# Kernel tuning notes

Measured on AMD Instinct MI355X. Metric: run time of the kernel, lower is better.

The kernel has to match this reference:

```python
import jax, jax.numpy as jnp
import numpy as np

D_X = 1024
D_TEXT = 768
FUSION_DIM = D_X + D_TEXT  # 1792
M = 16
K = 2


def setup_inputs() -> dict:
    key = jax.random.key(0)
    k1, k2, k3, k4, k5 = jax.random.split(key, 5)
    B, H, W = 256, 32, 32
    x = jax.random.normal(k1, (B, D_X, H, W), dtype=jnp.float32)
    degraded = jax.random.normal(k2, (B, D_TEXT), dtype=jnp.float32)
    # learned params (random so routing is non-trivial)
    w_fusion = jax.random.normal(k3, (FUSION_DIM, FUSION_DIM), dtype=jnp.float32) * (1.0 / np.sqrt(FUSION_DIM))
    b_fusion = jax.random.normal(k4, (FUSION_DIM,), dtype=jnp.float32) * 0.01
    w_gate = jax.random.normal(k5, (FUSION_DIM, M), dtype=jnp.float32) * 0.02
    return {"x": x, "degraded": degraded, "w_fusion": w_fusion,
            "b_fusion": b_fusion, "w_gate": w_gate}


def reference(x, degraded, w_fusion, b_fusion, w_gate):
    B = x.shape[0]
    # global average pool over H,W -> [B, d_x]
    x_pooled = jnp.mean(x, axis=(2, 3))
    fused = jnp.concatenate([x_pooled, degraded], axis=1)        # [B, d_x+d_text]
    fused = jnp.dot(fused, w_fusion) + b_fusion                  # Linear
    fused = jax.nn.gelu(fused, approximate=False)                # exact GELU (torch default)
    clean_logits = jnp.dot(fused, w_gate)                        # [B, M]
    probs_for_mi = jax.nn.softmax(clean_logits, axis=1)
    # eval path: logits = clean_logits (no noise)
    num_consider = min(K + 1, M)
    top_logits, top_indices = jax.lax.top_k(clean_logits, num_consider)
    top_k_logits = top_logits[:, :K]
    top_k_indices = top_indices[:, :K]
    top_k_gates = jax.nn.softmax(top_k_logits, axis=1)
    rows = jnp.arange(B)[:, None]
    gates = jnp.zeros_like(clean_logits).at[rows, top_k_indices].set(top_k_gates)
    moe_loss = jnp.float32(0.0)
    return gates, moe_loss, probs_for_mi, top_k_indices
```

## Files before the change

### kernel.cpp

```cpp
#include <hip/hip_runtime.h>
#include <math.h>

#define D_X      1024
#define D_TEXT   768
#define FDIM     1792
#define BATCH    256
#define M_EXP    16
#define HW_TOT   1024

#define OUT_GATES 0
#define OUT_LOSS  4096
#define OUT_PROBS 4097
#define OUT_IDX   8193

#define NBLK_DGEMM 224
#define NBLK_POOL  (BATCH * D_X / 4)

__global__ __launch_bounds__(256) void pool_deggemm_kernel(const float* __restrict__ x,
                                                           const float* __restrict__ deg,
                                                           const float* __restrict__ W,
                                                           float* __restrict__ fused,
                                                           float* __restrict__ pact2) {
    __shared__ float As1[32][33];
    __shared__ float Ws1[32][64];

    const int bid = blockIdx.x;
    const int tid = threadIdx.x;

    if (bid >= NBLK_DGEMM) {
        const int gtid = (bid - NBLK_DGEMM) * 256 + tid;
        const int row  = gtid >> 6;
        const int lane = gtid & 63;
        const float4* xr = reinterpret_cast<const float4*>(x + (size_t)row * HW_TOT);
        float s = 0.0f;
#pragma unroll
        for (int k = 0; k < 4; ++k) {
            float4 v = xr[k * 64 + lane];
            s += v.x + v.y + v.z + v.w;
        }
#pragma unroll
        for (int off = 32; off > 0; off >>= 1) s += __shfl_xor(s, off, 64);
        if (lane == 0) fused[row] = s * (1.0f / 1024.0f);
        return;
    }

    const int mb = bid / 28;
    const int nb = bid % 28;
    const int m0 = mb * 32;
    const int n0 = nb * 64;

    const int tx = tid & 15;
    const int ty = tid >> 4;

    const int ar  = tid >> 3;
    const int ak4 = (tid & 7) * 4;
    const int wk  = tid >> 4;
    const int wc4 = (tid & 15) * 4;

    float acc[2][4] = {};

    for (int k0 = 0; k0 < D_TEXT; k0 += 32) {
        __syncthreads();
        {
            const float4 a = *reinterpret_cast<const float4*>(
                deg + (size_t)(m0 + ar) * D_TEXT + k0 + ak4);
            As1[ak4 + 0][ar] = a.x; As1[ak4 + 1][ar] = a.y;
            As1[ak4 + 2][ar] = a.z; As1[ak4 + 3][ar] = a.w;
            *reinterpret_cast<float4*>(&Ws1[wk][wc4]) =
                *reinterpret_cast<const float4*>(W + (size_t)(D_X + k0 + wk) * FDIM + n0 + wc4);
            *reinterpret_cast<float4*>(&Ws1[wk + 16][wc4]) =
                *reinterpret_cast<const float4*>(W + (size_t)(D_X + k0 + wk + 16) * FDIM + n0 + wc4);
        }
        __syncthreads();
#pragma unroll
        for (int kk = 0; kk < 32; ++kk) {
            const float2 a = *reinterpret_cast<const float2*>(&As1[kk][ty * 2]);
            const float4 w = *reinterpret_cast<const float4*>(&Ws1[kk][tx * 4]);
            acc[0][0] = fmaf(a.x, w.x, acc[0][0]);
            acc[0][1] = fmaf(a.x, w.y, acc[0][1]);
            acc[0][2] = fmaf(a.x, w.z, acc[0][2]);
            acc[0][3] = fmaf(a.x, w.w, acc[0][3]);
            acc[1][0] = fmaf(a.y, w.x, acc[1][0]);
            acc[1][1] = fmaf(a.y, w.y, acc[1][1]);
            acc[1][2] = fmaf(a.y, w.z, acc[1][2]);
            acc[1][3] = fmaf(a.y, w.w, acc[1][3]);
        }
    }

#pragma unroll
    for (int i = 0; i < 2; ++i) {
        float4 v;
        v.x = acc[i][0]; v.y = acc[i][1]; v.z = acc[i][2]; v.w = acc[i][3];
        *reinterpret_cast<float4*>(pact2 + (size_t)(m0 + ty * 2 + i) * FDIM + n0 + tx * 4) = v;
    }
}

#define BM 32
#define BN 64
#define BK 64
#define KDIM D_X
#define NITER (KDIM / BK)
#define ASTR 36

#define AS(buf, k, m) As[(buf) * 2304 + (k) * ASTR + (m)]
#define WS(buf, k, n) Ws[(buf) * 4096 + (k) * 64 + (n)]
#define PACC(w, m, n) smem[(w) * 2048 + (m) * 64 + (n)]
#define ACTS(m, n)    smem[8192 + (m) * 65 + (n)]
#define WGS(n, e)     smem[10272 + (n) * M_EXP + (e)]

#define LOADA(k0)                                                                            \
    pa0 = *reinterpret_cast<const float4*>(A + (size_t)(m0 + ar) * KDIM + (k0) + ak4);       \
    pa1 = *reinterpret_cast<const float4*>(A + (size_t)(m0 + ar + 16) * KDIM + (k0) + ak4);

#define LOADW(k0)                                                                            \
    pw0 = *reinterpret_cast<const float4*>(W + (size_t)((k0) + wr0) * FDIM + n0 + wc4);      \
    pw1 = *reinterpret_cast<const float4*>(W + (size_t)((k0) + wr0 + 16) * FDIM + n0 + wc4); \
    pw2 = *reinterpret_cast<const float4*>(W + (size_t)((k0) + wr0 + 32) * FDIM + n0 + wc4); \
    pw3 = *reinterpret_cast<const float4*>(W + (size_t)((k0) + wr0 + 48) * FDIM + n0 + wc4);

#define STOREA(buf)                                                                          \
    AS(buf, ak4 + 0, ar) = pa0.x; AS(buf, ak4 + 1, ar) = pa0.y;                              \
    AS(buf, ak4 + 2, ar) = pa0.z; AS(buf, ak4 + 3, ar) = pa0.w;                              \
    AS(buf, ak4 + 0, ar + 16) = pa1.x; AS(buf, ak4 + 1, ar + 16) = pa1.y;                    \
    AS(buf, ak4 + 2, ar + 16) = pa1.z; AS(buf, ak4 + 3, ar + 16) = pa1.w;

#define STOREW(buf)                                                                          \
    *reinterpret_cast<float4*>(&WS(buf, wr0, wc4))      = pw0;                               \
    *reinterpret_cast<float4*>(&WS(buf, wr0 + 16, wc4)) = pw1;                               \
    *reinterpret_cast<float4*>(&WS(buf, wr0 + 32, wc4)) = pw2;                               \
    *reinterpret_cast<float4*>(&WS(buf, wr0 + 48, wc4)) = pw3;

__global__ __launch_bounds__(256) void gemm_gate_kernel(const float* __restrict__ A,
                                                        const float* __restrict__ W,
                                                        const float* __restrict__ pact2,
                                                        const float* __restrict__ bias,
                                                        const float* __restrict__ wg,
                                                        float* __restrict__ part,
                                                        int* __restrict__ done,
                                                        float* __restrict__ out) {
    __shared__ float smem[12800];
    __shared__ int isLast;
    float* As = smem;
    float* Ws = smem + 4608;

    const int tid = threadIdx.x;
    const int m0 = blockIdx.x * BM;
    const int n0 = blockIdx.y * BN;

    const int ar  = tid >> 4;
    const int ak4 = (tid & 15) * 4;
    const int wr0 = tid >> 4;
    const int wc4 = (tid & 15) * 4;

    const int wv   = tid >> 6;
    const int lane = tid & 63;
    const int mg   = lane >> 3;
    const int ng   = lane & 7;

    float4 pa0, pa1, pw0, pw1, pw2, pw3;

    LOADA(0); LOADW(0);
    STOREA(0); STOREW(0);
    LOADA(BK); LOADW(BK);
    __syncthreads();

    float acc[4][8] = {};
    int cur = 0;

    for (int t = 0; t < NITER; ++t) {
#pragma unroll
        for (int s = 0; s < 16; ++s) {
            const int kk = wv * 16 + s;
            const float4 a  = *reinterpret_cast<const float4*>(&AS(cur, kk, mg * 4));
            const float4 w0 = *reinterpret_cast<const float4*>(&WS(cur, kk, ng * 8));
            const float4 w1 = *reinterpret_cast<const float4*>(&WS(cur, kk, ng * 8 + 4));
            const float av[4] = {a.x, a.y, a.z, a.w};
            const float wvv[8] = {w0.x, w0.y, w0.z, w0.w, w1.x, w1.y, w1.z, w1.w};
#pragma unroll
            for (int i = 0; i < 4; ++i)
#pragma unroll
                for (int j = 0; j < 8; ++j)
                    acc[i][j] = fmaf(av[i], wvv[j], acc[i][j]);
        }
        if (t < NITER - 1) {
            const int nxt = cur ^ 1;
            STOREA(nxt); STOREW(nxt);
            if (t < NITER - 2) {
                const int k0 = (t + 2) * BK;
                LOADA(k0); LOADW(k0);
            }
            __syncthreads();
            cur = nxt;
        }
    }

    __syncthreads();

#pragma unroll
    for (int i = 0; i < 4; ++i) {
        float4 v0, v1;
        v0.x = acc[i][0]; v0.y = acc[i][1]; v0.z = acc[i][2]; v0.w = acc[i][3];
        v1.x = acc[i][4]; v1.y = acc[i][5]; v1.z = acc[i][6]; v1.w = acc[i][7];
        *reinterpret_cast<float4*>(&PACC(wv, mg * 4 + i, ng * 8))     = v0;
        *reinterpret_cast<float4*>(&PACC(wv, mg * 4 + i, ng * 8 + 4)) = v1;
    }
    {
        const int r  = tid >> 2;
        const int c4 = (tid & 3) * 4;
        *reinterpret_cast<float4*>(&WGS(r, c4)) =
            *reinterpret_cast<const float4*>(wg + (size_t)(n0 + r) * M_EXP + c4);
    }
    __syncthreads();

    {
        const int m   = tid >> 3;
        const int nb8 = (tid & 7) * 8;
#pragma unroll
        for (int h = 0; h < 2; ++h) {
            const int n = nb8 + h * 4;
            const float4 p  = *reinterpret_cast<const float4*>(
                pact2 + (size_t)(m0 + m) * FDIM + n0 + n);
            const float4 bb = *reinterpret_cast<const float4*>(bias + n0 + n);
            const float pv[4] = {p.x, p.y, p.z, p.w};
            const float bv[4] = {bb.x, bb.y, bb.z, bb.w};
#pragma unroll
            for (int j = 0; j < 4; ++j) {
                const float v = ((PACC(0, m, n + j) + PACC(1, m, n + j))
                               + (PACC(2, m, n + j) + PACC(3, m, n + j)))
                               + pv[j] + bv[j];
                ACTS(m, n + j) = v * 0.5f * (1.0f + erff(v * 0.70710678118654752440f));
            }
        }
    }
    __syncthreads();

    const int pm = tid >> 3;
    const int pe = (tid & 7) * 2;
    float s0 = 0.0f, s1 = 0.0f;
#pragma unroll
    for (int n = 0; n < BN; ++n) {
        const float a = ACTS(pm, n);
        s0 = fmaf(a, WGS(n, pe), s0);
        s1 = fmaf(a, WGS(n, pe + 1), s1);
    }
    float* pr = part + ((size_t)blockIdx.y * BATCH + m0 + pm) * M_EXP + pe;
    pr[0] = s0;
    pr[1] = s1;

    __threadfence();
    __syncthreads();
    if (tid == 0) {
        const int prev = __hip_atomic_fetch_add(done, 1, __ATOMIC_ACQ_REL,
                                                __HIP_MEMORY_SCOPE_AGENT);
        isLast = (prev == 8 * 28 - 1);
    }
    __syncthreads();
    if (!isLast) return;

    {
        const int b = tid;
        float l[M_EXP];
#pragma unroll
        for (int m = 0; m < M_EXP; ++m) l[m] = 0.0f;
        for (int nb2 = 0; nb2 < FDIM / BN; ++nb2) {
            const float4* prr = reinterpret_cast<const float4*>(
                part + ((size_t)nb2 * BATCH + b) * M_EXP);
#pragma unroll
            for (int q = 0; q < 4; ++q) {
                const float4 v = prr[q];
                l[q * 4 + 0] += v.x;
                l[q * 4 + 1] += v.y;
                l[q * 4 + 2] += v.z;
                l[q * 4 + 3] += v.w;
            }
        }
        float mx = l[0];
#pragma unroll
        for (int m = 1; m < M_EXP; ++m) mx = fmaxf(mx, l[m]);
        float e[M_EXP], s = 0.0f;
#pragma unroll
        for (int m = 0; m < M_EXP; ++m) { e[m] = expf(l[m] - mx); s += e[m]; }
        const float inv = 1.0f / s;
#pragma unroll
        for (int m = 0; m < M_EXP; ++m) out[OUT_PROBS + b * M_EXP + m] = e[m] * inv;

        int i0 = 0; float v0 = l[0];
#pragma unroll
        for (int m = 1; m < M_EXP; ++m) if (l[m] > v0) { v0 = l[m]; i0 = m; }
        int i1 = -1; float v1 = -INFINITY;
#pragma unroll
        for (int m = 0; m < M_EXP; ++m) if (m != i0 && l[m] > v1) { v1 = l[m]; i1 = m; }

        const float t = expf(v1 - v0);
        const float g0 = 1.0f / (1.0f + t);
        const float g1 = t * g0;
#pragma unroll
        for (int m = 0; m < M_EXP; ++m) out[OUT_GATES + b * M_EXP + m] = 0.0f;
        out[OUT_GATES + b * M_EXP + i0] = g0;
        out[OUT_GATES + b * M_EXP + i1] = g1;
        out[OUT_IDX + b * 2 + 0] = (float)i0;
        out[OUT_IDX + b * 2 + 1] = (float)i1;
        if (b == 0) out[OUT_LOSS] = 0.0f;
    }
}

extern "C" void kernel_launch(void* const* d_in, const int* in_sizes, int n_in,
                              void* d_out, int out_size, void* d_ws, size_t ws_size,
                              hipStream_t stream) {
    const float* x        = (const float*)d_in[0];
    const float* degraded = (const float*)d_in[1];
    const float* w_fusion = (const float*)d_in[2];
    const float* b_fusion = (const float*)d_in[3];
    const float* w_gate   = (const float*)d_in[4];
    float* out = (float*)d_out;

    float* fused = (float*)d_ws;
    float* pact2 = fused + (size_t)BATCH * D_X;
    float* part  = pact2 + (size_t)BATCH * FDIM;
    int*   done  = (int*)(part + (size_t)28 * BATCH * M_EXP);

    hipMemsetAsync(done, 0, sizeof(int), stream);

    pool_deggemm_kernel<<<NBLK_DGEMM + NBLK_POOL, 256, 0, stream>>>(x, degraded, w_fusion,
                                                                   fused, pact2);

    gemm_gate_kernel<<<dim3(BATCH / BM, FDIM / BN), 256, 0, stream>>>(fused, w_fusion, pact2,
                                                                     b_fusion, w_gate, part,
                                                                     done, out);
}
```

Baseline: 234.3 us.

## Split-K the pooled-feature GEMM across two blocks with per-tile completion counters

The main GEMM over the pooled x features is split into two K halves via a third grid dimension, doubling block count from 224 to 448. Each half writes partial sums to a global workspace, and a per-tile atomic counter lets the second finisher sum both halves, add the bias and degraded contribution, apply GELU, and run the gate projection. The intra-block 4-wave K split with shared-memory reduction is replaced by a simpler 2x4 per-thread tile. The aim is better CU occupancy on a small grid, at the cost of extra global traffic for partials and an added atomic synchronization.

```diff
diff --git a/kernel.cpp b/kernel.cpp
--- a/kernel.cpp
+++ b/kernel.cpp
@@ -98,15 +98,14 @@
 #define BM 32
 #define BN 64
 #define BK 64
+#define KHALF 512
+#define NITER (KHALF / BK)
 #define KDIM D_X
-#define NITER (KDIM / BK)
-#define ASTR 36
-
-#define AS(buf, k, m) As[(buf) * 2304 + (k) * ASTR + (m)]
-#define WS(buf, k, n) Ws[(buf) * 4096 + (k) * 64 + (n)]
-#define PACC(w, m, n) smem[(w) * 2048 + (m) * 64 + (n)]
-#define ACTS(m, n)    smem[8192 + (m) * 65 + (n)]
-#define WGS(n, e)     smem[10272 + (n) * M_EXP + (e)]
+
+#define AS(buf, k, m) smem[(buf) * 2112 + (k) * 33 + (m)]
+#define WS(buf, k, n) smem[4224 + (buf) * 4096 + (k) * 64 + (n)]
+#define ACTS(m, n)    smem[(m) * 65 + (n)]
+#define WGS(n, e)     smem[2080 + (n) * M_EXP + (e)]
 
 #define LOADA(k0)                                                                            \
     pa0 = *reinterpret_cast<const float4*>(A + (size_t)(m0 + ar) * KDIM + (k0) + ak4);       \
@@ -135,58 +134,56 @@
                                                         const float* __restrict__ pact2,
                                                         const float* __restrict__ bias,
                                                         const float* __restrict__ wg,
+                                                        float* __restrict__ pactz,
                                                         float* __restrict__ part,
+                                                        int* __restrict__ tilectr,
                                                         int* __restrict__ done,
                                                         float* __restrict__ out) {
-    __shared__ float smem[12800];
-    __shared__ int isLast;
-    float* As = smem;
-    float* Ws = smem + 4608;
+    __shared__ float smem[12416];
+    __shared__ int isL;
 
     const int tid = threadIdx.x;
     const int m0 = blockIdx.x * BM;
     const int n0 = blockIdx.y * BN;
-
+    const int z  = blockIdx.z;
+    const int kz = z * KHALF;
+
+    const int tx = tid & 15;
+    const int ty = tid >> 4;
     const int ar  = tid >> 4;
     const int ak4 = (tid & 15) * 4;
     const int wr0 = tid >> 4;
     const int wc4 = (tid & 15) * 4;
 
-    const int wv   = tid >> 6;
-    const int lane = tid & 63;
-    const int mg   = lane >> 3;
-    const int ng   = lane & 7;
-
     float4 pa0, pa1, pw0, pw1, pw2, pw3;
 
-    LOADA(0); LOADW(0);
+    LOADA(kz); LOADW(kz);
     STOREA(0); STOREW(0);
-    LOADA(BK); LOADW(BK);
-    __syncthreads();
-
-    float acc[4][8] = {};
+    LOADA(kz + BK); LOADW(kz + BK);
+    __syncthreads();
+
+    float acc[2][4] = {};
     int cur = 0;
 
     for (int t = 0; t < NITER; ++t) {
 #pragma unroll
-        for (int s = 0; s < 16; ++s) {
-            const int kk = wv * 16 + s;
-            const float4 a  = *reinterpret_cast<const float4*>(&AS(cur, kk, mg * 4));
-            const float4 w0 = *reinterpret_cast<const float4*>(&WS(cur, kk, ng * 8));
-            const float4 w1 = *reinterpret_cast<const float4*>(&WS(cur, kk, ng * 8 + 4));
-            const float av[4] = {a.x, a.y, a.z, a.w};
-            const float wvv[8] = {w0.x, w0.y, w0.z, w0.w, w1.x, w1.y, w1.z, w1.w};
-#pragma unroll
-            for (int i = 0; i < 4; ++i)
-#pragma unroll
-                for (int j = 0; j < 8; ++j)
-                    acc[i][j] = fmaf(av[i], wvv[j], acc[i][j]);
+        for (int kk = 0; kk < BK; ++kk) {
+            const float2 a = *reinterpret_cast<const float2*>(&AS(cur, kk, ty * 2));
+            const float4 w = *reinterpret_cast<const float4*>(&WS(cur, kk, tx * 4));
+            acc[0][0] = fmaf(a.x, w.x, acc[0][0]);
+            acc[0][1] = fmaf(a.x, w.y, acc[0][1]);
+            acc[0][2] = fmaf(a.x, w.z, acc[0][2]);
+            acc[0][3] = fmaf(a.x, w.w, acc[0][3]);
+            acc[1][0] = fmaf(a.y, w.x, acc[1][0]);
+            acc[1][1] = fmaf(a.y, w.y, acc[1][1]);
+            acc[1][2] = fmaf(a.y, w.z, acc[1][2]);
+            acc[1][3] = fmaf(a.y, w.w, acc[1][3]);
         }
         if (t < NITER - 1) {
             const int nxt = cur ^ 1;
             STOREA(nxt); STOREW(nxt);
             if (t < NITER - 2) {
-                const int k0 = (t + 2) * BK;
+                const int k0 = kz + (t + 2) * BK;
                 LOADA(k0); LOADW(k0);
             }
             __syncthreads();
@@ -194,15 +191,49 @@
         }
     }
 
-    __syncthreads();
-
-#pragma unroll
-    for (int i = 0; i < 4; ++i) {
-        float4 v0, v1;
-        v0.x = acc[i][0]; v0.y = acc[i][1]; v0.z = acc[i][2]; v0.w = acc[i][3];
-        v1.x = acc[i][4]; v1.y = acc[i][5]; v1.z = acc[i][6]; v1.w = acc[i][7];
-        *reinterpret_cast<float4*>(&PACC(wv, mg * 4 + i, ng * 8))     = v0;
-        *reinterpret_cast<float4*>(&PACC(wv, mg * 4 + i, ng * 8 + 4)) = v1;
+#pragma unroll
+    for (int i = 0; i < 2; ++i) {
+        float4 v;
+        v.x = acc[i][0]; v.y = acc[i][1]; v.z = acc[i][2]; v.w = acc[i][3];
+        *reinterpret_cast<float4*>(
+            pactz + ((size_t)z * BATCH + m0 + ty * 2 + i) * FDIM + n0 + tx * 4) = v;
+    }
+
+    __threadfence();
+    __syncthreads();
+    if (tid == 0) {
+        const int prev = __hip_atomic_fetch_add(&tilectr[blockIdx.x * 28 + blockIdx.y], 1,
+                                                __ATOMIC_ACQ_REL, __HIP_MEMORY_SCOPE_AGENT);
+        isL = (prev == 1);
+    }
+    __syncthreads();
+    if (!isL) return;
+
+    {
+        const int m  = tid >> 3;
+        const int n8 = (tid & 7) * 8;
+        const size_t rowoff = (size_t)(m0 + m) * FDIM + n0 + n8;
+        float vv[8];
+        {
+            const float4 q0 = *reinterpret_cast<const float4*>(pactz + rowoff);
+            const float4 q1 = *reinterpret_cast<const float4*>(pactz + rowoff + 4);
+            const float4 r0 = *reinterpret_cast<const float4*>(
+                pactz + (size_t)BATCH * FDIM + rowoff);
+            const float4 r1 = *reinterpret_cast<const float4*>(
+                pactz + (size_t)BATCH * FDIM + rowoff + 4);
+            const float4 p0 = *reinterpret_cast<const float4*>(pact2 + rowoff);
+            const float4 p1 = *reinterpret_cast<const float4*>(pact2 + rowoff + 4);
+            const float4 b0 = *reinterpret_cast<const float4*>(bias + n0 + n8);
+            const float4 b1 = *reinterpret_cast<const float4*>(bias + n0 + n8 + 4);
+            vv[0] = (q0.x + r0.x) + p0.x + b0.x; vv[1] = (q0.y + r0.y) + p0.y + b0.y;
+            vv[2] = (q0.z + r0.z) + p0.z + b0.z; vv[3] = (q0.w + r0.w) + p0.w + b0.w;
+            vv[4] = (q1.x + r1.x) + p1.x + b1.x; vv[5] = (q1.y + r1.y) + p1.y + b1.y;
+            vv[6] = (q1.z + r1.z) + p1.z + b1.z; vv[7] = (q1.w + r1.w) + p1.w + b1.w;
+        }
+        __syncthreads();
+#pragma unroll
+        for (int j = 0; j < 8; ++j)
+            ACTS(m, n8 + j) = vv[j] * 0.5f * (1.0f + erff(vv[j] * 0.70710678118654752440f));
     }
     {
         const int r  = tid >> 2;
@@ -212,28 +243,6 @@
     }
     __syncthreads();
 
-    {
-        const int m   = tid >> 3;
-        const int nb8 = (tid & 7) * 8;
-#pragma unroll
-        for (int h = 0; h < 2; ++h) {
-            const int n = nb8 + h * 4;
-            const float4 p  = *reinterpret_cast<const float4*>(
-                pact2 + (size_t)(m0 + m) * FDIM + n0 + n);
-            const float4 bb = *reinterpret_cast<const float4*>(bias + n0 + n);
-            const float pv[4] = {p.x, p.y, p.z, p.w};
-            const float bv[4] = {bb.x, bb.y, bb.z, bb.w};
-#pragma unroll
-            for (int j = 0; j < 4; ++j) {
-                const float v = ((PACC(0, m, n + j) + PACC(1, m, n + j))
-                               + (PACC(2, m, n + j) + PACC(3, m, n + j)))
-                               + pv[j] + bv[j];
-                ACTS(m, n + j) = v * 0.5f * (1.0f + erff(v * 0.70710678118654752440f));
-            }
-        }
-    }
-    __syncthreads();
-
     const int pm = tid >> 3;
     const int pe = (tid & 7) * 2;
     float s0 = 0.0f, s1 = 0.0f;
@@ -252,16 +261,16 @@
     if (tid == 0) {
         const int prev = __hip_atomic_fetch_add(done, 1, __ATOMIC_ACQ_REL,
                                                 __HIP_MEMORY_SCOPE_AGENT);
-        isLast = (prev == 8 * 28 - 1);
-    }
-    __syncthreads();
-    if (!isLast) return;
+        isL = (prev == 8 * 28 - 1);
+    }
+    __syncthreads();
+    if (!isL) return;
 
     {
         const int b = tid;
         float l[M_EXP];
 #pragma unroll
-        for (int m = 0; m < M_EXP; ++m) l[m] = 0.0f;
+        for (int mm = 0; mm < M_EXP; ++mm) l[mm] = 0.0f;
         for (int nb2 = 0; nb2 < FDIM / BN; ++nb2) {
             const float4* prr = reinterpret_cast<const float4*>(
                 part + ((size_t)nb2 * BATCH + b) * M_EXP);
@@ -276,26 +285,26 @@
         }
         float mx = l[0];
 #pragma unroll
-        for (int m = 1; m < M_EXP; ++m) mx = fmaxf(mx, l[m]);
+        for (int mm = 1; mm < M_EXP; ++mm) mx = fmaxf(mx, l[mm]);
         float e[M_EXP], s = 0.0f;
 #pragma unroll
-        for (int m = 0; m < M_EXP; ++m) { e[m] = expf(l[m] - mx); s += e[m]; }
+        for (int mm = 0; mm < M_EXP; ++mm) { e[mm] = expf(l[mm] - mx); s += e[mm]; }
         const float inv = 1.0f / s;
 #pragma unroll
-        for (int m = 0; m < M_EXP; ++m) out[OUT_PROBS + b * M_EXP + m] = e[m] * inv;
+        for (int mm = 0; mm < M_EXP; ++mm) out[OUT_PROBS + b * M_EXP + mm] = e[mm] * inv;
 
         int i0 = 0; float v0 = l[0];
 #pragma unroll
-        for (int m = 1; m < M_EXP; ++m) if (l[m] > v0) { v0 = l[m]; i0 = m; }
+        for (int mm = 1; mm < M_EXP; ++mm) if (l[mm] > v0) { v0 = l[mm]; i0 = mm; }
         int i1 = -1; float v1 = -INFINITY;
 #pragma unroll
-        for (int m = 0; m < M_EXP; ++m) if (m != i0 && l[m] > v1) { v1 = l[m]; i1 = m; }
+        for (int mm = 0; mm < M_EXP; ++mm) if (mm != i0 && l[mm] > v1) { v1 = l[mm]; i1 = mm; }
 
         const float t = expf(v1 - v0);
         const float g0 = 1.0f / (1.0f + t);
         const float g1 = t * g0;
 #pragma unroll
-        for (int m = 0; m < M_EXP; ++m) out[OUT_GATES + b * M_EXP + m] = 0.0f;
+        for (int mm = 0; mm < M_EXP; ++mm) out[OUT_GATES + b * M_EXP + mm] = 0.0f;
         out[OUT_GATES + b * M_EXP + i0] = g0;
         out[OUT_GATES + b * M_EXP + i1] = g1;
         out[OUT_IDX + b * 2 + 0] = (float)i0;
@@ -316,15 +325,16 @@
 
     float* fused = (float*)d_ws;
     float* pact2 = fused + (size_t)BATCH * D_X;
-    float* part  = pact2 + (size_t)BATCH * FDIM;
-    int*   done  = (int*)(part + (size_t)28 * BATCH * M_EXP);
-
-    hipMemsetAsync(done, 0, sizeof(int), stream);
+    float* pactz = pact2 + (size_t)BATCH * FDIM;
+    float* part  = pactz + (size_t)2 * BATCH * FDIM;
+    int*   ctrs  = (int*)(part + (size_t)28 * BATCH * M_EXP);
+
+    hipMemsetAsync(ctrs, 0, 225 * sizeof(int), stream);
 
     pool_deggemm_kernel<<<NBLK_DGEMM + NBLK_POOL, 256, 0, stream>>>(x, degraded, w_fusion,
                                                                    fused, pact2);
 
-    gemm_gate_kernel<<<dim3(BATCH / BM, FDIM / BN), 256, 0, stream>>>(fused, w_fusion, pact2,
-                                                                     b_fusion, w_gate, part,
-                                                                     done, out);
+    gemm_gate_kernel<<<dim3(8, 28, 2), 256, 0, stream>>>(fused, w_fusion, pact2,
+                                                         b_fusion, w_gate, pactz, part,
+                                                         ctrs, ctrs + 224, out);
 }
```

After: 295.1 us. +26.0%, slower.
